# Kernel optimization log

Hardware: AMD Instinct MI355X
Metric: run time of the kernel (lower is better)

Reference implementation:

```python
import jax, jax.numpy as jnp
import numpy as np
import math

N_HEADS = 16
D_MODEL = 1024
HEAD_DIM = D_MODEL // N_HEADS
ROPE_THETA = 10000.0


def _rope_cos_sin(seq_len, head_dim, dtype):
    # freqs = 1/theta^(2i/d), angles = outer(t, freqs)  -> [seq_len, head_dim//2]
    inv_freq = 1.0 / (ROPE_THETA ** (jnp.arange(0, head_dim, 2, dtype=jnp.float32) / head_dim))
    ang = jnp.arange(seq_len, dtype=jnp.float32)[:, None] * inv_freq[None, :]
    return jnp.cos(ang).astype(dtype), jnp.sin(ang).astype(dtype)


def _apply_rope(t, cos, sin):
    # t: [B, N, H, D]; treat last dim as complex pairs (a, b); multiply by e^{i*ang}
    B, N, H, D = t.shape
    tr = t.reshape(B, N, H, D // 2, 2)
    a, b = tr[..., 0], tr[..., 1]
    c = cos[None, :, None, :]  # [1, N, 1, D/2]
    s = sin[None, :, None, :]
    out = jnp.stack([a * c - b * s, a * s + b * c], axis=-1)
    return out.reshape(B, N, H, D)


def setup_inputs() -> dict:
    key = jax.random.key(0)
    ks = jax.random.split(key, 9)
    B, N, D = 4, 2048, D_MODEL
    scale = 0.02
    inp = {"x": jax.random.normal(ks[0], (B, N, D), dtype=jnp.float32)}
    for i, nm in enumerate(["q", "k", "v", "o"]):
        inp[f"w{nm}"] = jax.random.normal(ks[1 + 2 * i], (D, D), dtype=jnp.float32) * scale
        inp[f"b{nm}"] = jax.random.normal(ks[2 + 2 * i], (D,), dtype=jnp.float32) * scale
    return inp


def reference(x, wq, bq, wk, bk, wv, bv, wo, bo):
    B, N, D = x.shape
    H, Hd = N_HEADS, HEAD_DIM
    q = (x @ wq.T + bq).reshape(B, N, H, Hd)
    k = (x @ wk.T + bk).reshape(B, N, H, Hd)
    v = (x @ wv.T + bv).reshape(B, N, H, Hd)
    cos, sin = _rope_cos_sin(N, Hd, x.dtype)
    q = _apply_rope(q, cos, sin)
    k = _apply_rope(k, cos, sin)
    # SDPA, no mask, eval mode (dropout_p = 0)
    scores = jnp.einsum("bqhd,bkhd->bhqk", q, k) / math.sqrt(Hd)
    attn = jax.nn.softmax(scores, axis=-1)
    out = jnp.einsum("bhqk,bkhd->bqhd", attn, v)  # [B, N, H, Hd]
    out = out.reshape(B, N, D)
    return out @ wo.T + bo
```

## Files before the change

kernel.cpp:

```cpp
#include <hip/hip_runtime.h>
#include <math.h>
#include <stdint.h>

#define BBATCH 4
#define NTOK   2048
#define DMOD   1024
#define NH     16
#define HD     64
#define MTOT   8192

typedef __bf16 bf16;
typedef __bf16 bf16x2 __attribute__((ext_vector_type(2)));
typedef __bf16 bf16x4 __attribute__((ext_vector_type(4)));
typedef __bf16 bf16x8 __attribute__((ext_vector_type(8)));
typedef float  f32x4  __attribute__((ext_vector_type(4)));
typedef float  f32x16 __attribute__((ext_vector_type(16)));
typedef unsigned int u32;
typedef unsigned int u32x2 __attribute__((ext_vector_type(2)));
typedef unsigned int u32x4 __attribute__((ext_vector_type(4)));

typedef __attribute__((address_space(3))) unsigned int lds_u32;
typedef __attribute__((address_space(1))) unsigned int glb_u32;

__device__ __forceinline__ void gload16(const bf16* g, bf16* l) {
    __builtin_amdgcn_global_load_lds((glb_u32*)g, (lds_u32*)l, 16, 0, 0);
}

__device__ __forceinline__ u32 pack_bf16(float lo, float hi) {
    bf16x2 z; z[0] = (bf16)lo; z[1] = (bf16)hi;
    return __builtin_bit_cast(u32, z);
}

#define MFMA32(a, b, c) __builtin_amdgcn_mfma_f32_32x32x16_bf16((a), (b), (c), 0, 0, 0)

#define QSCALE 0.1803368801111204f

__global__ __launch_bounds__(256)
void convert_kernel(const float* __restrict__ x,  const float* __restrict__ wq,
                    const float* __restrict__ wk, const float* __restrict__ wv,
                    const float* __restrict__ wo,
                    bf16* __restrict__ xb,  bf16* __restrict__ wqb,
                    bf16* __restrict__ wkb, bf16* __restrict__ wvb,
                    bf16* __restrict__ wob,
                    float* __restrict__ ct, float* __restrict__ st)
{
    if (blockIdx.x < 256) {
        int idx = blockIdx.x * 256 + threadIdx.x;
        int n = idx >> 5, p = idx & 31;
        float inv = powf(10000.0f, -(float)(2 * p) / 64.0f);
        float ang = (float)n * inv;
        ct[idx] = cosf(ang);
        st[idx] = sinf(ang);
    }

    const int X4 = (MTOT * DMOD) / 4;
    const int W4 = (DMOD * DMOD) / 4;
    int i = blockIdx.x * 256 + threadIdx.x;
    const float* src; bf16* dst; int off;
    if (i < X4) { src = x; dst = xb; off = i; }
    else {
        int j = i - X4; int w = j / W4; off = j - w * W4;
        src = (w == 0) ? wq : (w == 1) ? wk : (w == 2) ? wv : wo;
        dst = (w == 0) ? wqb : (w == 1) ? wkb : (w == 2) ? wvb : wob;
    }
    float4 v = ((const float4*)src)[off];
    bf16x4 o;
    o[0] = (bf16)v.x; o[1] = (bf16)v.y; o[2] = (bf16)v.z; o[3] = (bf16)v.w;
    *(bf16x4*)(dst + (size_t)off * 4) = o;
}

__global__ __launch_bounds__(512)
void gemm_qkv(const bf16* __restrict__ A,
              const bf16* __restrict__ wq, const bf16* __restrict__ wk,
              const bf16* __restrict__ wv,
              const float* __restrict__ bq, const float* __restrict__ bk,
              const float* __restrict__ bv,
              bf16* __restrict__ qb, bf16* __restrict__ kb, bf16* __restrict__ vtb,
              const float* __restrict__ ct, const float* __restrict__ st)
{
    __shared__ __align__(16) bf16 As[2][256 * 32];
    __shared__ __align__(16) bf16 Bs[2][128 * 32];

    const int sel = blockIdx.x >> 3;
    const int n0  = (blockIdx.x & 7) * 128;
    const int m0  = blockIdx.y * 256;
    const bf16*  W    = (sel == 0) ? wq : (sel == 1) ? wk : wv;
    const float* bias = (sel == 0) ? bq : (sel == 1) ? bk : bv;
    bf16*        out  = (sel == 0) ? qb : (sel == 1) ? kb : vtb;

    const int tid = threadIdx.x;
    const int l   = tid & 63;
    const int wid = tid >> 6;
    const int wm  = wid >> 1, wn = wid & 1;
    const int fr  = l & 15, fg = l >> 4;

    const int srow  = tid >> 2;
    const int sslot = (tid & 3) ^ ((srow >> 1) & 3);
    const bf16* gA0 = A + (size_t)(m0 + srow) * 1024 + sslot * 8;
    const bf16* gB0 = W + (size_t)(n0 + srow) * 1024 + sslot * 8;

    const int aswz = (fg ^ ((fr >> 1) & 3)) * 8;
    int aoff[4], boff[4];
#pragma unroll
    for (int i = 0; i < 4; ++i) {
        aoff[i] = (wm * 64 + i * 16 + fr) * 32 + aswz;
        boff[i] = (wn * 64 + i * 16 + fr) * 32 + aswz;
    }

    f32x4 acc[4][4] = {};

#define QSTAGE(kt, b) do {                                           \
        const bf16* a0_ = gA0 + (kt) * 32;                           \
        const bf16* b0_ = gB0 + (kt) * 32;                           \
        gload16(a0_,                       As[b] + tid * 8);         \
        gload16(a0_ + (size_t)128 * 1024,  As[b] + 4096 + tid * 8);  \
        gload16(b0_,                       Bs[b] + tid * 8);         \
    } while (0)

    QSTAGE(0, 0);
    __syncthreads();
    int cur = 0;

    for (int kt = 0; kt < 32; ++kt) {
        if (kt < 31) QSTAGE(kt + 1, cur ^ 1);

        bf16x8 af[4], bfv[4];
#pragma unroll
        for (int i = 0; i < 4; ++i) af[i]  = *(const bf16x8*)(As[cur] + aoff[i]);
#pragma unroll
        for (int i = 0; i < 4; ++i) bfv[i] = *(const bf16x8*)(Bs[cur] + boff[i]);
#pragma unroll
        for (int mi = 0; mi < 4; ++mi)
#pragma unroll
            for (int ni = 0; ni < 4; ++ni)
                acc[mi][ni] = __builtin_amdgcn_mfma_f32_16x16x32_bf16(
                    af[mi], bfv[ni], acc[mi][ni], 0, 0, 0);

        __syncthreads();
        cur ^= 1;
    }
#undef QSTAGE

    if (sel == 2) {
#pragma unroll
        for (int ni = 0; ni < 4; ++ni) {
            const int col = n0 + wn * 64 + ni * 16 + fr;
            const int h = col >> 6, dd = col & 63;
            const float bvv = bias[col];
#pragma unroll
            for (int mi = 0; mi < 4; ++mi) {
                const int rowb = m0 + wm * 64 + mi * 16 + fg * 4;
                const int bi = rowb >> 11, npb = rowb & (NTOK - 1);
                bf16x4 ov;
#pragma unroll
                for (int r = 0; r < 4; ++r) ov[r] = (bf16)(acc[mi][ni][r] + bvv);
                *(bf16x4*)(out + ((size_t)(bi * NH + h) * HD + dd) * NTOK + npb) = ov;
            }
        }
    } else {
        const float scale = (sel == 0) ? QSCALE : 1.0f;
#pragma unroll
        for (int ni = 0; ni < 4; ++ni) {
            const int col = n0 + wn * 64 + ni * 16 + fr;
            const int h = col >> 6, dd = col & 63, p = (dd >> 1);
            const float bvv = bias[col];
#pragma unroll
            for (int mi = 0; mi < 4; ++mi) {
                const int rowb = m0 + wm * 64 + mi * 16 + fg * 4;
#pragma unroll
                for (int r = 0; r < 4; ++r) {
                    const int row = rowb + r;
                    const int bi = row >> 11, np = row & (NTOK - 1);
                    float v  = acc[mi][ni][r] + bvv;
                    float pv = __shfl_xor(v, 1);
                    float c = ct[np * 32 + p], s = st[np * 32 + p];
                    float o = (dd & 1) ? (pv * s + v * c) : (v * c - pv * s);
                    o *= scale;
                    out[((size_t)(bi * NH + h) * NTOK + np) * HD + dd] = (bf16)o;
                }
            }
        }
    }
}

__global__ __launch_bounds__(256)
void gemm_oproj(const bf16* __restrict__ A, const bf16* __restrict__ W,
                const float* __restrict__ bias, float* __restrict__ out)
{
    __shared__ __align__(16) bf16 As[2][128 * 32];
    __shared__ __align__(16) bf16 Bs[2][128 * 32];

    const int m0 = blockIdx.y * 128, n0 = blockIdx.x * 128;
    const int tid = threadIdx.x;
    const int l   = tid & 63;
    const int wid = tid >> 6;
    const int wm  = wid >> 1, wn = wid & 1;
    const int fr  = l & 15, fg = l >> 4;

    const int srow  = tid >> 2;
    const int sslot = (tid & 3) ^ ((srow >> 1) & 3);
    const bf16* gA0 = A + (size_t)(m0 + srow) * 1024 + sslot * 8;
    const bf16* gB0 = W + (size_t)(n0 + srow) * 1024 + sslot * 8;

    const int aswz = (fg ^ ((fr >> 1) & 3)) * 8;
    int aoff[4], boff[4];
#pragma unroll
    for (int i = 0; i < 4; ++i) {
        aoff[i] = (wm * 64 + i * 16 + fr) * 32 + aswz;
        boff[i] = (wn * 64 + i * 16 + fr) * 32 + aswz;
    }

    f32x4 acc[4][4] = {};

#define OSTAGE(kt, b) do {                                          \
        const bf16* a0_ = gA0 + (kt) * 32;                          \
        const bf16* b0_ = gB0 + (kt) * 32;                          \
        gload16(a0_,                      As[b] + tid * 8);         \
        gload16(a0_ + (size_t)64 * 1024,  As[b] + 2048 + tid * 8);  \
        gload16(b0_,                      Bs[b] + tid * 8);         \
        gload16(b0_ + (size_t)64 * 1024,  Bs[b] + 2048 + tid * 8);  \
    } while (0)

    OSTAGE(0, 0);
    __syncthreads();
    int cur = 0;

    for (int kt = 0; kt < 32; ++kt) {
        if (kt < 31) OSTAGE(kt + 1, cur ^ 1);

        bf16x8 af[4], bfv[4];
#pragma unroll
        for (int i = 0; i < 4; ++i) af[i]  = *(const bf16x8*)(As[cur] + aoff[i]);
#pragma unroll
        for (int i = 0; i < 4; ++i) bfv[i] = *(const bf16x8*)(Bs[cur] + boff[i]);
#pragma unroll
        for (int mi = 0; mi < 4; ++mi)
#pragma unroll
            for (int ni = 0; ni < 4; ++ni)
                acc[mi][ni] = __builtin_amdgcn_mfma_f32_16x16x32_bf16(
                    af[mi], bfv[ni], acc[mi][ni], 0, 0, 0);

        __syncthreads();
        cur ^= 1;
    }
#undef OSTAGE

#pragma unroll
    for (int ni = 0; ni < 4; ++ni) {
        const int col = n0 + wn * 64 + ni * 16 + fr;
        const float bv = bias[col];
#pragma unroll
        for (int mi = 0; mi < 4; ++mi) {
            const int rowb = m0 + wm * 64 + mi * 16 + fg * 4;
#pragma unroll
            for (int r = 0; r < 4; ++r)
                out[(size_t)(rowb + r) * 1024 + col] = acc[mi][ni][r] + bv;
        }
    }
}

__global__ __launch_bounds__(256)
void attn_mfma(const bf16* __restrict__ Q, const bf16* __restrict__ K,
               const bf16* __restrict__ Vt, bf16* __restrict__ out)
{
    __shared__ __align__(16) bf16 Ks[2][64 * 64];
    __shared__ __align__(16) bf16 Vs[2][64 * 64];

    const int tid = threadIdx.x;
    const int l   = tid & 63;
    const int wid = tid >> 6;
    const int lq  = l & 31;
    const int hi  = l >> 5;
    const int rx  = lq & 7;
    const int q0 = blockIdx.x * 128;
    const int bh = blockIdx.y;

    const bf16* Qb = Q  + (size_t)bh * NTOK * HD;
    const bf16* Kb = K  + (size_t)bh * NTOK * HD;
    const bf16* Vb = Vt + (size_t)bh * HD * NTOK;

    bf16x8 qf[4];
#pragma unroll
    for (int c = 0; c < 4; ++c)
        qf[c] = *(const bf16x8*)(Qb + (size_t)(q0 + wid * 32 + lq) * HD + c * 16 + hi * 8);

    bf16x8 ones;
#pragma unroll
    for (int i = 0; i < 8; ++i) ones[i] = (bf16)1.0f;

    const int srow  = tid >> 3;
    const int sslot = (tid & 7) ^ (srow & 7);
    const bf16* gK0 = Kb + (size_t)srow * HD + sslot * 8;
    const bf16* gV0 = Vb + (size_t)srow * NTOK + sslot * 8;

#define ASTAGE(t, b) do {                                          \
        const bf16* gK_ = gK0 + (size_t)(t) * 64 * HD;             \
        const bf16* gV_ = gV0 + (size_t)(t) * 64;                  \
        gload16(gK_,                      Ks[b] + tid * 8);        \
        gload16(gK_ + 32 * HD,            Ks[b] + 2048 + tid * 8); \
        gload16(gV_,                      Vs[b] + tid * 8);        \
        gload16(gV_ + (size_t)32 * NTOK,  Vs[b] + 2048 + tid * 8); \
    } while (0)

    f32x16 o0 = {}, o1 = {};
    f32x16 l4 = {};

    ASTAGE(0, 0);
    __syncthreads();
    int cur = 0;

    for (int t = 0; t < 32; ++t) {
        if (t < 31) ASTAGE(t + 1, cur ^ 1);
        const bf16* Kc = Ks[cur];
        const bf16* Vc = Vs[cur];

        f32x16 t0 = {}, t1 = {};
#pragma unroll
        for (int c = 0; c < 4; ++c) {
            const int slot = ((c * 2 + hi) ^ rx) * 8;
            bf16x8 kf0 = *(const bf16x8*)(Kc + lq * 64 + slot);
            bf16x8 kf1 = *(const bf16x8*)(Kc + (32 + lq) * 64 + slot);
            t0 = MFMA32(kf0, qf[c], t0);
            t1 = MFMA32(kf1, qf[c], t1);
        }

#pragma unroll
        for (int r = 0; r < 16; ++r) t0[r] = __builtin_amdgcn_exp2f(t0[r]);
#pragma unroll
        for (int r = 0; r < 16; ++r) t1[r] = __builtin_amdgcn_exp2f(t1[r]);

#pragma unroll
        for (int b = 0; b < 2; ++b) {
            const f32x16& tb = b ? t1 : t0;
#pragma unroll
            for (int kc = 0; kc < 2; ++kc) {
                const int a0 = kc ? 8 : 0;
                const int a1 = kc ? 12 : 4;
                u32 X  = pack_bf16(tb[a0],     tb[a0 + 1]);
                u32 Y  = pack_bf16(tb[a1],     tb[a1 + 1]);
                u32 X2 = pack_bf16(tb[a0 + 2], tb[a0 + 3]);
                u32 Y2 = pack_bf16(tb[a1 + 2], tb[a1 + 3]);
                u32x2 s0 = __builtin_amdgcn_permlane32_swap(X,  Y,  false, false);
                u32x2 s1 = __builtin_amdgcn_permlane32_swap(X2, Y2, false, false);
                u32x4 bw;
                bw[0] = s0[0]; bw[1] = s1[0]; bw[2] = s0[1]; bw[3] = s1[1];
                const bf16x8 pf = __builtin_bit_cast(bf16x8, bw);

                const int slot = (((b * 4 + kc * 2) + hi) ^ rx) * 8;
                bf16x8 vf0 = *(const bf16x8*)(Vc + lq * 64 + slot);
                bf16x8 vf1 = *(const bf16x8*)(Vc + (32 + lq) * 64 + slot);
                o0 = MFMA32(vf0, pf, o0);
                o1 = MFMA32(vf1, pf, o1);
                l4 = MFMA32(ones, pf, l4);
            }
        }

        __syncthreads();
        cur ^= 1;
    }
#undef ASTAGE

    const int b_ = bh >> 4, h = bh & 15;
    const float inv = 1.0f / l4[0];
    const int token = q0 + wid * 32 + lq;
    bf16* dst = out + (size_t)(b_ * NTOK + token) * DMOD + h * HD;
#pragma unroll
    for (int dblk = 0; dblk < 2; ++dblk) {
        const f32x16& ob = dblk ? o1 : o0;
#pragma unroll
        for (int g = 0; g < 4; ++g) {
            bf16x4 ov;
#pragma unroll
            for (int r2 = 0; r2 < 4; ++r2) ov[r2] = (bf16)(ob[g * 4 + r2] * inv);
            *(bf16x4*)(dst + dblk * 32 + g * 8 + hi * 4) = ov;
        }
    }
}

extern "C" void kernel_launch(void* const* d_in, const int* in_sizes, int n_in,
                              void* d_out, int out_size, void* d_ws, size_t ws_size,
                              hipStream_t stream)
{
    (void)in_sizes; (void)n_in; (void)out_size; (void)ws_size;

    const float* x  = (const float*)d_in[0];
    const float* wq = (const float*)d_in[1];
    const float* bq = (const float*)d_in[2];
    const float* wk = (const float*)d_in[3];
    const float* bk = (const float*)d_in[4];
    const float* wv = (const float*)d_in[5];
    const float* bv = (const float*)d_in[6];
    const float* wo = (const float*)d_in[7];
    const float* bo = (const float*)d_in[8];
    float* out = (float*)d_out;

    const size_t XSZ = (size_t)MTOT * DMOD;
    const size_t WSZ = (size_t)DMOD * DMOD;
    bf16* xb  = (bf16*)d_ws;
    bf16* wqb = xb  + XSZ;
    bf16* wkb = wqb + WSZ;
    bf16* wvb = wkb + WSZ;
    bf16* wob = wvb + WSZ;
    bf16* qb  = wob + WSZ;
    bf16* kb  = qb  + XSZ;
    bf16* vtb = kb  + XSZ;
    bf16* ab  = vtb + XSZ;
    float* ct = (float*)(ab + XSZ);
    float* st = ct + (size_t)NTOK * 32;

    convert_kernel<<<dim3(12288), dim3(256), 0, stream>>>(x, wq, wk, wv, wo,
                                                          xb, wqb, wkb, wvb, wob,
                                                          ct, st);

    gemm_qkv<<<dim3(24, MTOT / 256), dim3(512), 0, stream>>>(
        xb, wqb, wkb, wvb, bq, bk, bv, qb, kb, vtb, ct, st);

    attn_mfma<<<dim3(NTOK / 128, BBATCH * NH), dim3(256), 0, stream>>>(qb, kb, vtb, ab);

    gemm_oproj<<<dim3(DMOD / 128, MTOT / 128), dim3(256), 0, stream>>>(ab, wob, bo, out);
}
```

Measured before the change: 321.4 us.

## Process two query tiles per warp in attention, reusing K/V fragments

Each warp now handles 64 query rows instead of 32, so every K and V fragment read from shared memory feeds two sets of MFMAs and the grid halves to 512 blocks. The softmax row sum is now accumulated with scalar adds plus a cross-half shuffle rather than an extra MFMA against a ones vector. Launch bounds request two blocks per CU. In exchange, register pressure roughly doubles for the accumulators, and the smaller grid gives fewer waves to hide latency.

```diff
diff --git a/kernel.cpp b/kernel.cpp
--- a/kernel.cpp
+++ b/kernel.cpp
@@ -29,6 +29,15 @@
 __device__ __forceinline__ u32 pack_bf16(float lo, float hi) {
     bf16x2 z; z[0] = (bf16)lo; z[1] = (bf16)hi;
     return __builtin_bit_cast(u32, z);
+}
+
+__device__ __forceinline__ float vsum16(f32x16 v) {
+    float a0 = v[0] + v[1],   a1 = v[2] + v[3];
+    float a2 = v[4] + v[5],   a3 = v[6] + v[7];
+    float a4 = v[8] + v[9],   a5 = v[10] + v[11];
+    float a6 = v[12] + v[13], a7 = v[14] + v[15];
+    float b0 = a0 + a1, b1 = a2 + a3, b2 = a4 + a5, b3 = a6 + a7;
+    return (b0 + b1) + (b2 + b3);
 }
 
 #define MFMA32(a, b, c) __builtin_amdgcn_mfma_f32_32x32x16_bf16((a), (b), (c), 0, 0, 0)
@@ -259,7 +268,7 @@
     }
 }
 
-__global__ __launch_bounds__(256)
+__global__ __launch_bounds__(256, 2)
 void attn_mfma(const bf16* __restrict__ Q, const bf16* __restrict__ K,
                const bf16* __restrict__ Vt, bf16* __restrict__ out)
 {
@@ -272,21 +281,20 @@
     const int lq  = l & 31;
     const int hi  = l >> 5;
     const int rx  = lq & 7;
-    const int q0 = blockIdx.x * 128;
+    const int q0 = blockIdx.x * 256;
     const int bh = blockIdx.y;
 
     const bf16* Qb = Q  + (size_t)bh * NTOK * HD;
     const bf16* Kb = K  + (size_t)bh * NTOK * HD;
     const bf16* Vb = Vt + (size_t)bh * HD * NTOK;
 
-    bf16x8 qf[4];
-#pragma unroll
-    for (int c = 0; c < 4; ++c)
-        qf[c] = *(const bf16x8*)(Qb + (size_t)(q0 + wid * 32 + lq) * HD + c * 16 + hi * 8);
-
-    bf16x8 ones;
-#pragma unroll
-    for (int i = 0; i < 8; ++i) ones[i] = (bf16)1.0f;
+    const int qbase = q0 + wid * 64;
+    bf16x8 qf0[4], qf1[4];
+#pragma unroll
+    for (int c = 0; c < 4; ++c) {
+        qf0[c] = *(const bf16x8*)(Qb + (size_t)(qbase + lq) * HD + c * 16 + hi * 8);
+        qf1[c] = *(const bf16x8*)(Qb + (size_t)(qbase + 32 + lq) * HD + c * 16 + hi * 8);
+    }
 
     const int srow  = tid >> 3;
     const int sslot = (tid & 7) ^ (srow & 7);
@@ -302,8 +310,9 @@
         gload16(gV_ + (size_t)32 * NTOK,  Vs[b] + 2048 + tid * 8); \
     } while (0)
 
-    f32x16 o0 = {}, o1 = {};
-    f32x16 l4 = {};
+    f32x16 oA0 = {}, oA1 = {};
+    f32x16 oB0 = {}, oB1 = {};
+    float lsA = 0.f, lsB = 0.f;
 
     ASTAGE(0, 0);
     __syncthreads();
@@ -314,45 +323,91 @@
         const bf16* Kc = Ks[cur];
         const bf16* Vc = Vs[cur];
 
-        f32x16 t0 = {}, t1 = {};
+        bf16x8 kf0[4], kf1[4];
 #pragma unroll
         for (int c = 0; c < 4; ++c) {
             const int slot = ((c * 2 + hi) ^ rx) * 8;
-            bf16x8 kf0 = *(const bf16x8*)(Kc + lq * 64 + slot);
-            bf16x8 kf1 = *(const bf16x8*)(Kc + (32 + lq) * 64 + slot);
-            t0 = MFMA32(kf0, qf[c], t0);
-            t1 = MFMA32(kf1, qf[c], t1);
-        }
-
-#pragma unroll
-        for (int r = 0; r < 16; ++r) t0[r] = __builtin_amdgcn_exp2f(t0[r]);
-#pragma unroll
-        for (int r = 0; r < 16; ++r) t1[r] = __builtin_amdgcn_exp2f(t1[r]);
-
-#pragma unroll
-        for (int b = 0; b < 2; ++b) {
-            const f32x16& tb = b ? t1 : t0;
-#pragma unroll
-            for (int kc = 0; kc < 2; ++kc) {
-                const int a0 = kc ? 8 : 0;
-                const int a1 = kc ? 12 : 4;
-                u32 X  = pack_bf16(tb[a0],     tb[a0 + 1]);
-                u32 Y  = pack_bf16(tb[a1],     tb[a1 + 1]);
-                u32 X2 = pack_bf16(tb[a0 + 2], tb[a0 + 3]);
-                u32 Y2 = pack_bf16(tb[a1 + 2], tb[a1 + 3]);
-                u32x2 s0 = __builtin_amdgcn_permlane32_swap(X,  Y,  false, false);
-                u32x2 s1 = __builtin_amdgcn_permlane32_swap(X2, Y2, false, false);
-                u32x4 bw;
-                bw[0] = s0[0]; bw[1] = s1[0]; bw[2] = s0[1]; bw[3] = s1[1];
-                const bf16x8 pf = __builtin_bit_cast(bf16x8, bw);
-
-                const int slot = (((b * 4 + kc * 2) + hi) ^ rx) * 8;
-                bf16x8 vf0 = *(const bf16x8*)(Vc + lq * 64 + slot);
-                bf16x8 vf1 = *(const bf16x8*)(Vc + (32 + lq) * 64 + slot);
-                o0 = MFMA32(vf0, pf, o0);
-                o1 = MFMA32(vf1, pf, o1);
-                l4 = MFMA32(ones, pf, l4);
-            }
+            kf0[c] = *(const bf16x8*)(Kc + lq * 64 + slot);
+            kf1[c] = *(const bf16x8*)(Kc + (32 + lq) * 64 + slot);
+        }
+
+        bf16x8 pfA[4], pfB[4];
+
+        {
+            f32x16 t0 = {}, t1 = {};
+#pragma unroll
+            for (int c = 0; c < 4; ++c) {
+                t0 = MFMA32(kf0[c], qf0[c], t0);
+                t1 = MFMA32(kf1[c], qf0[c], t1);
+            }
+#pragma unroll
+            for (int r = 0; r < 16; ++r) t0[r] = __builtin_amdgcn_exp2f(t0[r]);
+#pragma unroll
+            for (int r = 0; r < 16; ++r) t1[r] = __builtin_amdgcn_exp2f(t1[r]);
+            lsA += vsum16(t0) + vsum16(t1);
+#pragma unroll
+            for (int b = 0; b < 2; ++b) {
+                const f32x16& tb = b ? t1 : t0;
+#pragma unroll
+                for (int kc = 0; kc < 2; ++kc) {
+                    const int a0 = kc ? 8 : 0, a1 = kc ? 12 : 4;
+                    u32 X  = pack_bf16(tb[a0],     tb[a0 + 1]);
+                    u32 Y  = pack_bf16(tb[a1],     tb[a1 + 1]);
+                    u32 X2 = pack_bf16(tb[a0 + 2], tb[a0 + 3]);
+                    u32 Y2 = pack_bf16(tb[a1 + 2], tb[a1 + 3]);
+                    u32x2 s0 = __builtin_amdgcn_permlane32_swap(X,  Y,  false, false);
+                    u32x2 s1 = __builtin_amdgcn_permlane32_swap(X2, Y2, false, false);
+                    u32x4 bw;
+                    bw[0] = s0[0]; bw[1] = s1[0]; bw[2] = s0[1]; bw[3] = s1[1];
+                    pfA[b * 2 + kc] = __builtin_bit_cast(bf16x8, bw);
+                }
+            }
+        }
+
+        {
+            f32x16 t0 = {}, t1 = {};
+#pragma unroll
+            for (int c = 0; c < 4; ++c) {
+                t0 = MFMA32(kf0[c], qf1[c], t0);
+                t1 = MFMA32(kf1[c], qf1[c], t1);
+            }
+#pragma unroll
+            for (int r = 0; r < 16; ++r) t0[r] = __builtin_amdgcn_exp2f(t0[r]);
+#pragma unroll
+            for (int r = 0; r < 16; ++r) t1[r] = __builtin_amdgcn_exp2f(t1[r]);
+            lsB += vsum16(t0) + vsum16(t1);
+#pragma unroll
+            for (int b = 0; b < 2; ++b) {
+                const f32x16& tb = b ? t1 : t0;
+#pragma unroll
+                for (int kc = 0; kc < 2; ++kc) {
+                    const int a0 = kc ? 8 : 0, a1 = kc ? 12 : 4;
+                    u32 X  = pack_bf16(tb[a0],     tb[a0 + 1]);
+                    u32 Y  = pack_bf16(tb[a1],     tb[a1 + 1]);
+                    u32 X2 = pack_bf16(tb[a0 + 2], tb[a0 + 3]);
+                    u32 Y2 = pack_bf16(tb[a1 + 2], tb[a1 + 3]);
+                    u32x2 s0 = __builtin_amdgcn_permlane32_swap(X,  Y,  false, false);
+                    u32x2 s1 = __builtin_amdgcn_permlane32_swap(X2, Y2, false, false);
+                    u32x4 bw;
+                    bw[0] = s0[0]; bw[1] = s1[0]; bw[2] = s0[1]; bw[3] = s1[1];
+                    pfB[b * 2 + kc] = __builtin_bit_cast(bf16x8, bw);
+                }
+            }
+        }
+
+        bf16x8 vf0[4], vf1[4];
+#pragma unroll
+        for (int j = 0; j < 4; ++j) {
+            const int slot = ((j * 2 + hi) ^ rx) * 8;
+            vf0[j] = *(const bf16x8*)(Vc + lq * 64 + slot);
+            vf1[j] = *(const bf16x8*)(Vc + (32 + lq) * 64 + slot);
+        }
+#pragma unroll
+        for (int j = 0; j < 4; ++j) {
+            oA0 = MFMA32(vf0[j], pfA[j], oA0);
+            oA1 = MFMA32(vf1[j], pfA[j], oA1);
+            oB0 = MFMA32(vf0[j], pfB[j], oB0);
+            oB1 = MFMA32(vf1[j], pfB[j], oB1);
         }
 
         __syncthreads();
@@ -361,18 +416,39 @@
 #undef ASTAGE
 
     const int b_ = bh >> 4, h = bh & 15;
-    const float inv = 1.0f / l4[0];
-    const int token = q0 + wid * 32 + lq;
-    bf16* dst = out + (size_t)(b_ * NTOK + token) * DMOD + h * HD;
-#pragma unroll
-    for (int dblk = 0; dblk < 2; ++dblk) {
-        const f32x16& ob = dblk ? o1 : o0;
-#pragma unroll
-        for (int g = 0; g < 4; ++g) {
-            bf16x4 ov;
-#pragma unroll
-            for (int r2 = 0; r2 < 4; ++r2) ov[r2] = (bf16)(ob[g * 4 + r2] * inv);
-            *(bf16x4*)(dst + dblk * 32 + g * 8 + hi * 4) = ov;
+    const float lA = lsA + __shfl_xor(lsA, 32);
+    const float lB = lsB + __shfl_xor(lsB, 32);
+    const float invA = 1.0f / lA;
+    const float invB = 1.0f / lB;
+
+    {
+        const int token = qbase + lq;
+        bf16* dst = out + (size_t)(b_ * NTOK + token) * DMOD + h * HD;
+#pragma unroll
+        for (int dblk = 0; dblk < 2; ++dblk) {
+            const f32x16& ob = dblk ? oA1 : oA0;
+#pragma unroll
+            for (int g = 0; g < 4; ++g) {
+                bf16x4 ov;
+#pragma unroll
+                for (int r2 = 0; r2 < 4; ++r2) ov[r2] = (bf16)(ob[g * 4 + r2] * invA);
+                *(bf16x4*)(dst + dblk * 32 + g * 8 + hi * 4) = ov;
+            }
+        }
+    }
+    {
+        const int token = qbase + 32 + lq;
+        bf16* dst = out + (size_t)(b_ * NTOK + token) * DMOD + h * HD;
+#pragma unroll
+        for (int dblk = 0; dblk < 2; ++dblk) {
+            const f32x16& ob = dblk ? oB1 : oB0;
+#pragma unroll
+            for (int g = 0; g < 4; ++g) {
+                bf16x4 ov;
+#pragma unroll
+                for (int r2 = 0; r2 < 4; ++r2) ov[r2] = (bf16)(ob[g * 4 + r2] * invB);
+                *(bf16x4*)(dst + dblk * 32 + g * 8 + hi * 4) = ov;
+            }
         }
     }
 }
@@ -415,7 +491,7 @@
     gemm_qkv<<<dim3(24, MTOT / 256), dim3(512), 0, stream>>>(
         xb, wqb, wkb, wvb, bq, bk, bv, qb, kb, vtb, ct, st);
 
-    attn_mfma<<<dim3(NTOK / 128, BBATCH * NH), dim3(256), 0, stream>>>(qb, kb, vtb, ab);
+    attn_mfma<<<dim3(NTOK / 256, BBATCH * NH), dim3(256), 0, stream>>>(qb, kb, vtb, ab);
 
     gemm_oproj<<<dim3(DMOD / 128, MTOT / 128), dim3(256), 0, stream>>>(ab, wob, bo, out);
 }
```

Result: faster. 297.4 us (-7.5%).
